# Optimization experiments

Hardware: AMD Instinct MI355X
Metric: run time of the kernel (lower is better)

## Reference

```python
import jax, jax.numpy as jnp
import numpy as np

N = 50000
E = 1600000
D_IN = 64
D_H = 64
D_EMB = 64
D_DEC = 128
B = 4096


def setup_inputs() -> dict:
    key = jax.random.key(0)
    ks = jax.random.split(key, 16)
    def lin(k, fan_in, fan_out):
        return jax.random.normal(k, (fan_in, fan_out), jnp.float32) / np.sqrt(fan_in)
    inp = {
        "x": jax.random.normal(ks[0], (N, D_IN), jnp.float32),
        "edge_index": jax.random.randint(ks[1], (2, E), 0, N),
        "drug_index": jax.random.randint(ks[2], (B, 2), 1, N),
        "bn_gamma": jnp.ones((D_IN,), jnp.float32),
        "bn_beta": jnp.zeros((D_IN,), jnp.float32),
        "Wu1": lin(ks[3], D_IN, D_H), "Wd1": lin(ks[4], D_IN, D_H), "Wb1": lin(ks[5], D_IN, D_H),
        "Wu2": lin(ks[6], 3 * D_H, D_H), "Wd2": lin(ks[7], 3 * D_H, D_H), "Wb2": lin(ks[8], 3 * D_H, D_H),
        "Wu3": lin(ks[9], 3 * D_H, D_EMB), "Wd3": lin(ks[10], 3 * D_H, D_EMB), "Wb3": lin(ks[11], 3 * D_H, D_EMB),
        "P1": jax.random.normal(ks[12], (3 * D_EMB, D_DEC), jnp.float32),
        "P2": jax.random.normal(ks[13], (D_DEC, D_DEC), jnp.float32),
    }
    return inp


def _batchnorm(x, gamma, beta, eps=1e-5):
    mu = jnp.mean(x, axis=0)
    var = jnp.var(x, axis=0)  # biased, matches torch BN training normalization
    return gamma * (x - mu) / jnp.sqrt(var + eps) + beta


def _bgnn_conv(x, row, col, Wu, Wd, Wb, n_nodes):
    # up direction: messages flow row -> col (source_to_target)
    up = x @ Wu
    dn = x @ Wd
    bi = x @ Wb
    ones = jnp.ones(row.shape[0], x.dtype)
    deg_up = jax.ops.segment_sum(ones, col, num_segments=n_nodes)  # in-degree at col
    x_up = jax.ops.segment_sum(up[row] / deg_up[col][:, None], col, num_segments=n_nodes)
    # down direction: flipped edge_index -> messages flow col -> row
    deg_dn = jax.ops.segment_sum(ones, row, num_segments=n_nodes)
    x_dn = jax.ops.segment_sum(dn[col] / deg_dn[row][:, None], row, num_segments=n_nodes)
    c = jnp.concatenate([x_up, x_dn, bi], axis=-1)
    nrm = jnp.linalg.norm(c, axis=-1, keepdims=True)
    return c / jnp.maximum(nrm, 1e-12)


def _leaky(t):
    return jnp.where(t >= 0, t, 0.1 * t)


def reference(x, edge_index, drug_index, bn_gamma, bn_beta,
              Wu1, Wd1, Wb1, Wu2, Wd2, Wb2, Wu3, Wd3, Wb3, P1, P2):
    row, col = edge_index[0], edge_index[1]
    h = _batchnorm(x, bn_gamma, bn_beta)
    h = _leaky(_bgnn_conv(h, row, col, Wu1, Wd1, Wb1, N))
    h = _leaky(_bgnn_conv(h, row, col, Wu2, Wd2, Wb2, N))
    h = _leaky(_bgnn_conv(h, row, col, Wu3, Wd3, Wb3, N))
    di = jnp.reshape(drug_index, (-1, 2))
    a = h[di[:, 0] - 1]  # [B, 3*D_EMB]
    b = h[di[:, 1] - 1]
    M = P1 @ P2 @ P1.T  # [3*D_EMB, 3*D_EMB]
    ypred = jnp.einsum('bd,de,be->b', a, M, b)[:, None]
    return ypred
```

## Files before the change

kernel.cpp:

```cpp
#include <hip/hip_runtime.h>

#define PN 50000
#define PE 1600000
#define PB 4096
#define NP 8
#define PSZ 6250
#define NSW 4
#define SWSZ 12500
#define SCAP 210000
#define CCAP 60000
#define NSL2 4
#define GBLK 2048
#define NPER 7

typedef __attribute__((ext_vector_type(8))) short bf16x8;
typedef __attribute__((ext_vector_type(4))) float f32x4;

__device__ inline float b2f(ushort u) {
    union { unsigned int i; float f; } x; x.i = ((unsigned int)u) << 16; return x.f;
}
__device__ inline ushort f2b(float f) {
    union { float f; unsigned int i; } x; x.f = f;
    unsigned int r = (x.i + 0x7FFFu + ((x.i >> 16) & 1u)) >> 16;
    return (ushort)r;
}

static constexpr size_t L4N = 4 * (size_t)PN;
static constexpr size_t IDXCAP3 = PE + 3 * L4N + 1024;
static constexpr size_t OFF_BN     = 0;
static constexpr size_t OFF_GCUR   = 256;
static constexpr size_t OFF_CCUR   = 272;
static constexpr size_t OFF_TMPM   = 336;
static constexpr size_t OFF_M      = OFF_TMPM + 192 * 128;
static constexpr size_t OFF_WOFFU  = OFF_M + 192 * 192;
static constexpr size_t OFF_WOFFD  = OFF_WOFFU + L4N + 4;
static constexpr size_t OFF_WDEGU  = OFF_WOFFD + L4N + 4;
static constexpr size_t OFF_WDEGD  = OFF_WDEGU + L4N;
static constexpr size_t OFF_PHISTU = OFF_WDEGD + L4N;
static constexpr size_t OFF_PHISTD = OFF_PHISTU + NSL2 * L4N;
static constexpr size_t OFF_IDXU   = OFF_PHISTD + NSL2 * L4N;
static constexpr size_t OFF_IDXD   = OFF_IDXU + (IDXCAP3 + 1) / 2;
static constexpr size_t OFF_STGU   = OFF_IDXD + (IDXCAP3 + 1) / 2;
static constexpr size_t OFF_STGD   = OFF_STGU + NP * (size_t)SCAP;
static constexpr size_t OFF_CHK    = OFF_STGD + NP * (size_t)SCAP;
static constexpr size_t OFF_WB16   = OFF_CHK + 64 * (size_t)CCAP;
static constexpr size_t OFF_HB     = OFF_WB16 + 43008;
static constexpr size_t OFF_PROJ   = OFF_HB + (size_t)PN * 96;

__global__ __launch_bounds__(256) void bn_stats_kernel(const float* __restrict__ x,
                                                       float* __restrict__ sums, int N) {
    __shared__ float ls[256], ls2[256];
    int col = threadIdx.x & 63;
    int rstart = blockIdx.x * 4 + (threadIdx.x >> 6);
    float s = 0.f, s2 = 0.f;
    for (int r = rstart; r < N; r += gridDim.x * 4) {
        float v = x[(size_t)r * 64 + col];
        s += v; s2 += v * v;
    }
    ls[threadIdx.x] = s; ls2[threadIdx.x] = s2;
    __syncthreads();
    if (threadIdx.x < 64) {
        s  = ls[threadIdx.x]  + ls[threadIdx.x + 64]  + ls[threadIdx.x + 128]  + ls[threadIdx.x + 192];
        s2 = ls2[threadIdx.x] + ls2[threadIdx.x + 64] + ls2[threadIdx.x + 128] + ls2[threadIdx.x + 192];
        atomicAdd(&sums[col], s);
        atomicAdd(&sums[64 + col], s2);
    }
}

__global__ __launch_bounds__(64) void bn_finalize_kernel(const float* __restrict__ gamma,
                                                         const float* __restrict__ beta,
                                                         float* __restrict__ bn, int N) {
    int c = threadIdx.x;
    float mean = bn[c] / (float)N;
    float var = bn[64 + c] / (float)N - mean * mean;
    float sc = gamma[c] * rsqrtf(var + 1e-5f);
    bn[128 + c] = sc;
    bn[192 + c] = beta[c] - mean * sc;
}

__global__ __launch_bounds__(256) void bin_kernel(const int* __restrict__ ei,
                                                  int* __restrict__ gcur,
                                                  uint* __restrict__ stgu,
                                                  uint* __restrict__ stgd, int E) {
    __shared__ uint sbuf[16][1024];
    __shared__ int scnt[16], sbase[16];
    const int tid = threadIdx.x;
    for (int base = blockIdx.x * 1024; base < E; base += gridDim.x * 1024) {
        if (tid < 16) scnt[tid] = 0;
        __syncthreads();
#pragma unroll
        for (int j = 0; j < 4; ++j) {
            int e = base + j * 256 + tid;
            if (e < E) {
                int r = __builtin_nontemporal_load(&ei[e]);
                int c = __builtin_nontemporal_load(&ei[E + e]);
                int pu = c / PSZ;
                int slot = atomicAdd(&scnt[pu], 1);
                sbuf[pu][slot] = ((uint)c << 16) | (uint)r;
                int pd = r / PSZ;
                int slot2 = atomicAdd(&scnt[8 + pd], 1);
                sbuf[8 + pd][slot2] = ((uint)r << 16) | (uint)c;
            }
        }
        __syncthreads();
        if (tid < 16) sbase[tid] = atomicAdd(&gcur[tid], scnt[tid]);
        __syncthreads();
#pragma unroll 1
        for (int k = 0; k < 16; ++k) {
            int cnt = scnt[k];
            int gb = sbase[k];
            uint* dst = (k < 8) ? (stgu + (size_t)k * SCAP) : (stgd + (size_t)(k - 8) * SCAP);
            for (int i = tid; i < cnt; i += 256) {
                int gi = gb + i;
                if (gi < SCAP) dst[gi] = sbuf[k][i];
            }
        }
        __syncthreads();
    }
}

__global__ __launch_bounds__(256) void rebin_kernel(const uint* __restrict__ stgu,
                                                    const uint* __restrict__ stgd,
                                                    const int* __restrict__ gcur,
                                                    int* __restrict__ ccur,
                                                    uint* __restrict__ chk) {
    __shared__ uint sb[4][1024];
    __shared__ int sc[4], sbase[4];
    const int p = blockIdx.x & 7;
    const int dir = (blockIdx.x >> 3) & 1;
    const int sl = blockIdx.x >> 4;
    const int tid = threadIdx.x;
    const int cnt = min(gcur[dir * 8 + p], SCAP);
    const uint* stg = (dir ? stgd : stgu) + (size_t)p * SCAP;
    const int cbase = p + dir * 8;
    const int per = (cnt + 7) / 8;
    const int s0 = sl * per, s1 = min(cnt, s0 + per);
    for (int base = s0; base < s1; base += 1024) {
        if (tid < 4) sc[tid] = 0;
        __syncthreads();
#pragma unroll
        for (int j = 0; j < 4; ++j) {
            int i = base + j * 256 + tid;
            if (i < s1) {
                uint u = stg[i];
                int w = (int)(u & 0xFFFFu) / SWSZ;
                int slot = atomicAdd(&sc[w], 1);
                sb[w][slot] = u;
            }
        }
        __syncthreads();
        if (tid < 4) sbase[tid] = atomicAdd(&ccur[cbase + 16 * tid], sc[tid]);
        __syncthreads();
#pragma unroll 1
        for (int k = 0; k < 4; ++k) {
            int ck = sc[k];
            int gb = sbase[k];
            uint* dst = chk + (size_t)(cbase + 16 * k) * CCAP;
            for (int i = tid; i < ck; i += 256) {
                int gi = gb + i;
                if (gi < CCAP) dst[gi] = sb[k][i];
            }
        }
        __syncthreads();
    }
}

__global__ __launch_bounds__(256) void hist_kernel(const uint* __restrict__ chk,
                                                   const int* __restrict__ ccur,
                                                   int* __restrict__ phistu,
                                                   int* __restrict__ phistd) {
    __shared__ int hist[PSZ];
    const int c = blockIdx.x & 63;
    const int s = blockIdx.x >> 6;
    const int p = c & 7;
    const int dir = (c >> 3) & 1;
    const int w = c >> 4;
    const int tid = threadIdx.x;
    const int lo = p * PSZ;
    for (int i = tid; i < PSZ; i += 256) hist[i] = 0;
    __syncthreads();
    const int cnt = min(ccur[c], CCAP);
    const uint* stg = chk + (size_t)c * CCAP;
    const int per = (cnt + NSL2 - 1) / NSL2;
    const int s0 = s * per, s1 = min(cnt, s0 + per);
    for (int i = s0 + tid; i < s1; i += 256)
        atomicAdd(&hist[(int)(stg[i] >> 16) - lo], 1);
    __syncthreads();
    int* ph = (dir ? phistd : phistu) + (size_t)s * L4N;
    for (int i = tid; i < PSZ; i += 256) ph[(size_t)(lo + i) * NSW + w] = hist[i];
}

__global__ __launch_bounds__(1024) void scan_kernel(const int* __restrict__ phA,
                                                    const int* __restrict__ phB,
                                                    int* __restrict__ offA,
                                                    int* __restrict__ offB,
                                                    int* __restrict__ degA,
                                                    int* __restrict__ degB, int len) {
    const int* ph = blockIdx.x ? phB : phA;
    int* off = blockIdx.x ? offB : offA;
    int* dego = blockIdx.x ? degB : degA;
    __shared__ int wsum[17];
    int tid = threadIdx.x, lane = tid & 63, wid = tid >> 6;
    int run = 0;
    for (int base = 0; base < len; base += 4096) {
        int i4 = base + tid * 4;
        int4 v = make_int4(0, 0, 0, 0);
        if (i4 < len) {
#pragma unroll
            for (int sl = 0; sl < NSL2; ++sl) {
                int4 t = *(const int4*)&ph[(size_t)sl * len + i4];
                v.x += t.x; v.y += t.y; v.z += t.z; v.w += t.w;
            }
            *(int4*)&dego[i4] = v;
        }
        v.x = (v.x + 3) & ~3; v.y = (v.y + 3) & ~3;
        v.z = (v.z + 3) & ~3; v.w = (v.w + 3) & ~3;
        int lsum = v.x + v.y + v.z + v.w;
        int inc = lsum;
#pragma unroll
        for (int d = 1; d < 64; d <<= 1) {
            int t = __shfl_up(inc, d);
            if (lane >= d) inc += t;
        }
        if (lane == 63) wsum[wid] = inc;
        __syncthreads();
        if (tid == 0) {
            int r2 = 0;
#pragma unroll
            for (int i = 0; i < 16; ++i) { int t = wsum[i]; wsum[i] = r2; r2 += t; }
            wsum[16] = r2;
        }
        __syncthreads();
        if (i4 < len) {
            int pre = run + wsum[wid] + inc - lsum;
            int4 o;
            o.x = pre; o.y = pre + v.x; o.z = o.y + v.y; o.w = o.z + v.z;
            *(int4*)&off[i4] = o;
        }
        run += wsum[16];
        __syncthreads();
    }
    if (tid == 0) off[len] = run;
}

__global__ __launch_bounds__(256) void scatter_kernel(const uint* __restrict__ chk,
                                                      const int* __restrict__ ccur,
                                                      const int* __restrict__ phistu,
                                                      const int* __restrict__ phistd,
                                                      const int* __restrict__ woffu,
                                                      const int* __restrict__ woffd,
                                                      ushort* __restrict__ idxu,
                                                      ushort* __restrict__ idxd) {
    __shared__ int cur[PSZ];
    const int c = blockIdx.x & 63;
    const int s = blockIdx.x >> 6;
    const int p = c & 7;
    const int dir = (c >> 3) & 1;
    const int w = c >> 4;
    const int tid = threadIdx.x;
    const int lo = p * PSZ;
    const int* woff = (dir ? woffd : woffu);
    const int* phist = (dir ? phistd : phistu);
    for (int i = tid; i < PSZ; i += 256) {
        size_t key = (size_t)(lo + i) * NSW + w;
        int cv = woff[key];
        for (int t = 0; t < s; ++t) cv += phist[(size_t)t * L4N + key];
        cur[i] = cv;
    }
    __syncthreads();
    const int cnt = min(ccur[c], CCAP);
    const uint* stg = chk + (size_t)c * CCAP;
    ushort* idx = (dir ? idxd : idxu);
    const int per = (cnt + NSL2 - 1) / NSL2;
    const int s0 = s * per, s1 = min(cnt, s0 + per);
    for (int i = s0 + tid; i < s1; i += 256) {
        uint u = stg[i];
        int pos = atomicAdd(&cur[(int)(u >> 16) - lo], 1);
        idx[pos] = (ushort)(u & 0xFFFFu);
    }
}

template<int K>
__global__ __launch_bounds__(256) void wconv_kernel(const float* __restrict__ Wu,
                                                    const float* __restrict__ Wd,
                                                    const float* __restrict__ Wb,
                                                    ushort* __restrict__ out) {
    int idx = blockIdx.x * 256 + threadIdx.x;
    if (idx >= 192 * K) return;
    int c = idx / K, k = idx - c * K;
    const float* W = (c < 64) ? Wu : (c < 128 ? Wd : Wb);
    out[idx] = f2b(W[k * 64 + (c & 63)]);
}

template<int K, bool BN>
__global__ __launch_bounds__(256) void gemm_kernel(const ushort* __restrict__ hb,
                                                   const float* __restrict__ x,
                                                   const float* __restrict__ bn,
                                                   const ushort* __restrict__ wb,
                                                   ushort* __restrict__ proj, int nrows) {
    constexpr int KP = K + 8;
    __shared__ ushort wlds[192 * KP];
    const int tid = threadIdx.x;
    constexpr int KB8 = K / 8;
    for (int idx = tid; idx < 192 * KB8; idx += 256) {
        int col = idx / KB8, kb = idx - col * KB8;
        *(bf16x8*)&wlds[col * KP + kb * 8] = *(const bf16x8*)&wb[(size_t)col * K + kb * 8];
    }
    __syncthreads();
    const int lane = tid & 63, wid = tid >> 6;
    const int kgrp = (lane >> 4) * 8;
    const int rbase = blockIdx.x * 128 + wid * 32;
    int ar[2] = { min(rbase + (lane & 15), nrows - 1),
                  min(rbase + 16 + (lane & 15), nrows - 1) };
    f32x4 acc[2][12];
#pragma unroll
    for (int rt = 0; rt < 2; ++rt)
#pragma unroll
        for (int ct = 0; ct < 12; ++ct) acc[rt][ct] = (f32x4)0.0f;

#pragma unroll
    for (int k0 = 0; k0 < K; k0 += 32) {
        bf16x8 af[2];
        if (BN) {
#pragma unroll
            for (int rt = 0; rt < 2; ++rt)
#pragma unroll
                for (int j = 0; j < 8; ++j) {
                    int c = k0 + kgrp + j;
                    float v = x[(size_t)ar[rt] * 64 + c] * bn[128 + c] + bn[192 + c];
                    af[rt][j] = (short)f2b(v);
                }
        } else {
#pragma unroll
            for (int rt = 0; rt < 2; ++rt)
                af[rt] = *(const bf16x8*)&hb[(size_t)ar[rt] * 192 + k0 + kgrp];
        }
#pragma unroll
        for (int ct = 0; ct < 12; ++ct) {
            bf16x8 bfr = *(const bf16x8*)&wlds[(ct * 16 + (lane & 15)) * KP + k0 + kgrp];
            acc[0][ct] = __builtin_amdgcn_mfma_f32_16x16x32_bf16(af[0], bfr, acc[0][ct], 0, 0, 0);
            acc[1][ct] = __builtin_amdgcn_mfma_f32_16x16x32_bf16(af[1], bfr, acc[1][ct], 0, 0, 0);
        }
    }
    const int orow0 = blockIdx.x * 128 + wid * 32 + (lane >> 4) * 4;
#pragma unroll
    for (int rt = 0; rt < 2; ++rt)
#pragma unroll
        for (int ct = 0; ct < 12; ++ct) {
            int ocol = ct * 16 + (lane & 15);
#pragma unroll
            for (int j = 0; j < 4; ++j) {
                int orow = orow0 + rt * 16 + j;
                if (orow < nrows) proj[(size_t)orow * 192 + ocol] = f2b(acc[rt][ct][j]);
            }
        }
}

__global__ __launch_bounds__(256) void gather_kernel(const ushort* __restrict__ proj,
                                                     const int* __restrict__ woffu,
                                                     const int* __restrict__ wdegu,
                                                     const int* __restrict__ woffd,
                                                     const int* __restrict__ wdegd,
                                                     const ushort* __restrict__ idxu,
                                                     const ushort* __restrict__ idxd,
                                                     ushort* __restrict__ hb, int N) {
    const int gw = blockIdx.x * 4 + (threadIdx.x >> 6);
    const int nwaves = gridDim.x * 4;
    const int lane = threadIdx.x & 63;
    const int half = lane >> 5;
    const int sl = lane & 31;
    const int* __restrict__ woff = half ? woffd : woffu;
    const int* __restrict__ wdeg = half ? wdegd : wdegu;
    const ushort* __restrict__ idx = half ? idxd : idxu;
    const uint* __restrict__ rowb = (const uint*)proj + half * 32 + sl;

    float a0[NPER], a1[NPER];
    int dtot[NPER];
#pragma unroll
    for (int j = 0; j < NPER; ++j) { a0[j] = 0.f; a1[j] = 0.f; dtot[j] = 0; }

    for (int w = 0; w < NSW; ++w) {
#pragma unroll
        for (int j = 0; j < NPER; ++j) {
            int n = gw + j * nwaves;
            if (n < N) {
                int key = n * NSW + w;
                int s = woff[key];
                int cnt = wdeg[key];
                dtot[j] += cnt;
                const ushort* p = idx + s;
                for (int i = 0; i < cnt; i += 4) {
                    ushort4 U = *(const ushort4*)(p + i);
                    int v1 = (i + 1 < cnt), v2 = (i + 2 < cnt), v3 = (i + 3 < cnt);
                    int s0 = (int)U.x;
                    int s1 = v1 ? (int)U.y : 0;
                    int s2 = v2 ? (int)U.z : 0;
                    int s3 = v3 ? (int)U.w : 0;
                    uint w0 = rowb[(size_t)s0 * 96];
                    uint w1 = rowb[(size_t)s1 * 96];
                    uint w2 = rowb[(size_t)s2 * 96];
                    uint w3 = rowb[(size_t)s3 * 96];
                    if (!v1) w1 = 0; if (!v2) w2 = 0; if (!v3) w3 = 0;
                    a0[j] += __uint_as_float(w0 << 16) + __uint_as_float(w1 << 16)
                           + __uint_as_float(w2 << 16) + __uint_as_float(w3 << 16);
                    a1[j] += __uint_as_float(w0 & 0xFFFF0000u) + __uint_as_float(w1 & 0xFFFF0000u)
                           + __uint_as_float(w2 & 0xFFFF0000u) + __uint_as_float(w3 & 0xFFFF0000u);
                }
            }
        }
        __syncthreads();
    }

    uint* hb32 = (uint*)hb;
#pragma unroll
    for (int j = 0; j < NPER; ++j) {
        int n = gw + j * nwaves;
        if (n >= N) continue;
        float sc = 1.0f / (float)max(dtot[j], 1);
        float A0 = a0[j] * sc, A1 = a1[j] * sc;
        uint bw = (half == 0) ? ((const uint*)proj)[(size_t)n * 96 + 64 + sl] : 0u;
        float b0 = __uint_as_float(bw << 16);
        float b1 = __uint_as_float(bw & 0xFFFF0000u);
        float ss = A0 * A0 + A1 * A1 + b0 * b0 + b1 * b1;
#pragma unroll
        for (int off = 32; off; off >>= 1) ss += __shfl_xor(ss, off);
        float r = 1.0f / fmaxf(sqrtf(ss), 1e-12f);
        A0 *= r; A1 *= r; b0 *= r; b1 *= r;
        A0 = A0 >= 0.f ? A0 : 0.1f * A0;
        A1 = A1 >= 0.f ? A1 : 0.1f * A1;
        hb32[(size_t)n * 96 + half * 32 + sl] = (uint)f2b(A0) | ((uint)f2b(A1) << 16);
        if (half == 0) {
            b0 = b0 >= 0.f ? b0 : 0.1f * b0;
            b1 = b1 >= 0.f ? b1 : 0.1f * b1;
            hb32[(size_t)n * 96 + 64 + sl] = (uint)f2b(b0) | ((uint)f2b(b1) << 16);
        }
    }
}

__global__ __launch_bounds__(128) void m1_kernel(const float* __restrict__ P1,
                                                 const float* __restrict__ P2,
                                                 float* __restrict__ tmpM) {
    int i = blockIdx.x, c = threadIdx.x;
    float s = 0.f;
    for (int k = 0; k < 128; ++k) s += P1[i * 128 + k] * P2[k * 128 + c];
    tmpM[i * 128 + c] = s;
}

__global__ __launch_bounds__(192) void m2_kernel(const float* __restrict__ tmpM,
                                                 const float* __restrict__ P1,
                                                 float* __restrict__ M) {
    __shared__ float trow[128];
    int i = blockIdx.x, j = threadIdx.x;
    if (j < 128) trow[j] = tmpM[i * 128 + j];
    __syncthreads();
    float s = 0.f;
    for (int k = 0; k < 128; ++k) s += trow[k] * P1[j * 128 + k];
    M[i * 192 + j] = s;
}

__global__ __launch_bounds__(192) void decode_kernel(const ushort* __restrict__ hb,
                                                     const int* __restrict__ di,
                                                     const float* __restrict__ M,
                                                     float* __restrict__ out) {
    __shared__ alignas(16) float bvs[8][192];
    __shared__ float red[3][8];
    int pb = blockIdx.x * 8;
    int i = threadIdx.x;
#pragma unroll
    for (int p = 0; p < 8; ++p) {
        int nb = di[(pb + p) * 2 + 1] - 1;
        bvs[p][i] = b2f(hb[(size_t)nb * 192 + i]);
    }
    __syncthreads();
    float t[8] = {};
    const float4* M4 = (const float4*)(M + (size_t)i * 192);
    for (int j4 = 0; j4 < 48; ++j4) {
        float4 m = M4[j4];
#pragma unroll
        for (int p = 0; p < 8; ++p) {
            float4 b = *(const float4*)&bvs[p][j4 * 4];
            t[p] += m.x * b.x + m.y * b.y + m.z * b.z + m.w * b.w;
        }
    }
    int wid = i >> 6, lane = i & 63;
#pragma unroll
    for (int p = 0; p < 8; ++p) {
        int na = di[(pb + p) * 2] - 1;
        float v = b2f(hb[(size_t)na * 192 + i]) * t[p];
#pragma unroll
        for (int off = 32; off; off >>= 1) v += __shfl_xor(v, off);
        if (lane == 0) red[wid][p] = v;
    }
    __syncthreads();
    if (i < 8) out[pb + i] = red[0][i] + red[1][i] + red[2][i];
}

extern "C" void kernel_launch(void* const* d_in, const int* in_sizes, int n_in,
                              void* d_out, int out_size, void* d_ws, size_t ws_size,
                              hipStream_t stream) {
    const float* x     = (const float*)d_in[0];
    const int*   ei    = (const int*)d_in[1];
    const int*   di    = (const int*)d_in[2];
    const float* gamma = (const float*)d_in[3];
    const float* beta  = (const float*)d_in[4];
    const float* Wu[3] = {(const float*)d_in[5], (const float*)d_in[8],  (const float*)d_in[11]};
    const float* Wd[3] = {(const float*)d_in[6], (const float*)d_in[9],  (const float*)d_in[12]};
    const float* Wb[3] = {(const float*)d_in[7], (const float*)d_in[10], (const float*)d_in[13]};
    const float* P1    = (const float*)d_in[14];
    const float* P2    = (const float*)d_in[15];
    float* out = (float*)d_out;
    float* ws  = (float*)d_ws;

    float* bn    = ws + OFF_BN;
    int* gcur  = (int*)(ws + OFF_GCUR);
    int* ccur  = (int*)(ws + OFF_CCUR);
    float* tmpM  = ws + OFF_TMPM;
    float* M     = ws + OFF_M;
    int* woffu = (int*)(ws + OFF_WOFFU);
    int* woffd = (int*)(ws + OFF_WOFFD);
    int* wdegu = (int*)(ws + OFF_WDEGU);
    int* wdegd = (int*)(ws + OFF_WDEGD);
    int* phistu = (int*)(ws + OFF_PHISTU);
    int* phistd = (int*)(ws + OFF_PHISTD);
    ushort* idxu = (ushort*)(ws + OFF_IDXU);
    ushort* idxd = (ushort*)(ws + OFF_IDXD);
    uint* stgu = (uint*)(ws + OFF_STGU);
    uint* stgd = (uint*)(ws + OFF_STGD);
    uint* chk  = (uint*)(ws + OFF_CHK);
    ushort* wb16 = (ushort*)(ws + OFF_WB16);
    ushort* hb   = (ushort*)(ws + OFF_HB);
    ushort* proj = (ushort*)(ws + OFF_PROJ);
    ushort* wbl[3] = {wb16, wb16 + 12288, wb16 + 49152};

    hipMemsetAsync(ws, 0, 336 * sizeof(float), stream);

    bn_stats_kernel<<<200, 256, 0, stream>>>(x, bn, PN);
    bn_finalize_kernel<<<1, 64, 0, stream>>>(gamma, beta, bn, PN);

    bin_kernel<<<512, 256, 0, stream>>>(ei, gcur, stgu, stgd, PE);
    rebin_kernel<<<128, 256, 0, stream>>>(stgu, stgd, gcur, ccur, chk);
    hist_kernel<<<64 * NSL2, 256, 0, stream>>>(chk, ccur, phistu, phistd);
    scan_kernel<<<2, 1024, 0, stream>>>(phistu, phistd, woffu, woffd, wdegu, wdegd, (int)L4N);
    scatter_kernel<<<64 * NSL2, 256, 0, stream>>>(chk, ccur, phistu, phistd,
                                                  woffu, woffd, idxu, idxd);

    wconv_kernel<64><<<(192 * 64 + 255) / 256, 256, 0, stream>>>(Wu[0], Wd[0], Wb[0], wbl[0]);
    wconv_kernel<192><<<(192 * 192 + 255) / 256, 256, 0, stream>>>(Wu[1], Wd[1], Wb[1], wbl[1]);
    wconv_kernel<192><<<(192 * 192 + 255) / 256, 256, 0, stream>>>(Wu[2], Wd[2], Wb[2], wbl[2]);

    const int ngb = (PN + 127) / 128;
    gemm_kernel<64, true><<<ngb, 256, 0, stream>>>(hb, x, bn, wbl[0], proj, PN);
    gather_kernel<<<GBLK, 256, 0, stream>>>(proj, woffu, wdegu, woffd, wdegd, idxu, idxd, hb, PN);
    gemm_kernel<192, false><<<ngb, 256, 0, stream>>>(hb, x, bn, wbl[1], proj, PN);
    gather_kernel<<<GBLK, 256, 0, stream>>>(proj, woffu, wdegu, woffd, wdegd, idxu, idxd, hb, PN);
    gemm_kernel<192, false><<<ngb, 256, 0, stream>>>(hb, x, bn, wbl[2], proj, PN);
    gather_kernel<<<GBLK, 256, 0, stream>>>(proj, woffu, wdegu, woffd, wdegd, idxu, idxd, hb, PN);

    m1_kernel<<<192, 128, 0, stream>>>(P1, P2, tmpM);
    m2_kernel<<<192, 192, 0, stream>>>(tmpM, P1, M);
    decode_kernel<<<PB / 8, 192, 0, stream>>>(hb, di, M, out);
}
```

Measured before the change: 699.5 us.

## Single-pass edge binning, 8-wide padded gathers, and decode-only final aggregation

Merges the two-pass bin/rebin edge partitioning into one kernel that bins directly into 64 chunk buckets, using a small shared-memory buffer and a direct global atomic fallback on overflow. Pads each per-node index segment to a multiple of 8 with a sentinel node whose projection row is zeroed, so the gather loop reads 8 indices per step without validity masks. The last-layer aggregation now runs only for the nodes referenced by drug_index rather than all N nodes. This removes a staging pass and most of the last gather. In exchange it adds a padfill kernel, more index memory, and contended global atomics when a bucket overflows.

After: 655.2 us. 6.3% less time.

```diff
diff --git a/kernel.cpp b/kernel.cpp
--- a/kernel.cpp
+++ b/kernel.cpp
@@ -7,14 +7,17 @@
 #define PSZ 6250
 #define NSW 4
 #define SWSZ 12500
-#define SCAP 210000
 #define CCAP 60000
+#define BCAP 128
 #define NSL2 4
 #define GBLK 2048
 #define NPER 7
+#define GBLK3 512
+#define NPER3 4
 
 typedef __attribute__((ext_vector_type(8))) short bf16x8;
 typedef __attribute__((ext_vector_type(4))) float f32x4;
+typedef __attribute__((ext_vector_type(8))) unsigned short u16x8;
 
 __device__ inline float b2f(ushort u) {
     union { unsigned int i; float f; } x; x.i = ((unsigned int)u) << 16; return x.f;
@@ -26,10 +29,9 @@
 }
 
 static constexpr size_t L4N = 4 * (size_t)PN;
-static constexpr size_t IDXCAP3 = PE + 3 * L4N + 1024;
+static constexpr size_t IDXCAP = PE + 7 * L4N + 1024;
 static constexpr size_t OFF_BN     = 0;
-static constexpr size_t OFF_GCUR   = 256;
-static constexpr size_t OFF_CCUR   = 272;
+static constexpr size_t OFF_CCUR   = 256;
 static constexpr size_t OFF_TMPM   = 336;
 static constexpr size_t OFF_M      = OFF_TMPM + 192 * 128;
 static constexpr size_t OFF_WOFFU  = OFF_M + 192 * 192;
@@ -39,10 +41,8 @@
 static constexpr size_t OFF_PHISTU = OFF_WDEGD + L4N;
 static constexpr size_t OFF_PHISTD = OFF_PHISTU + NSL2 * L4N;
 static constexpr size_t OFF_IDXU   = OFF_PHISTD + NSL2 * L4N;
-static constexpr size_t OFF_IDXD   = OFF_IDXU + (IDXCAP3 + 1) / 2;
-static constexpr size_t OFF_STGU   = OFF_IDXD + (IDXCAP3 + 1) / 2;
-static constexpr size_t OFF_STGD   = OFF_STGU + NP * (size_t)SCAP;
-static constexpr size_t OFF_CHK    = OFF_STGD + NP * (size_t)SCAP;
+static constexpr size_t OFF_IDXD   = OFF_IDXU + (IDXCAP + 1) / 2;
+static constexpr size_t OFF_CHK    = OFF_IDXD + (IDXCAP + 1) / 2;
 static constexpr size_t OFF_WB16   = OFF_CHK + 64 * (size_t)CCAP;
 static constexpr size_t OFF_HB     = OFF_WB16 + 43008;
 static constexpr size_t OFF_PROJ   = OFF_HB + (size_t)PN * 96;
@@ -79,14 +79,13 @@
 }
 
 __global__ __launch_bounds__(256) void bin_kernel(const int* __restrict__ ei,
-                                                  int* __restrict__ gcur,
-                                                  uint* __restrict__ stgu,
-                                                  uint* __restrict__ stgd, int E) {
-    __shared__ uint sbuf[16][1024];
-    __shared__ int scnt[16], sbase[16];
+                                                  int* __restrict__ ccur,
+                                                  uint* __restrict__ chk, int E) {
+    __shared__ uint sbuf[64][BCAP];
+    __shared__ int scnt[64], sbase[64];
     const int tid = threadIdx.x;
     for (int base = blockIdx.x * 1024; base < E; base += gridDim.x * 1024) {
-        if (tid < 16) scnt[tid] = 0;
+        if (tid < 64) scnt[tid] = 0;
         __syncthreads();
 #pragma unroll
         for (int j = 0; j < 4; ++j) {
@@ -94,71 +93,29 @@
             if (e < E) {
                 int r = __builtin_nontemporal_load(&ei[e]);
                 int c = __builtin_nontemporal_load(&ei[E + e]);
-                int pu = c / PSZ;
-                int slot = atomicAdd(&scnt[pu], 1);
-                sbuf[pu][slot] = ((uint)c << 16) | (uint)r;
-                int pd = r / PSZ;
-                int slot2 = atomicAdd(&scnt[8 + pd], 1);
-                sbuf[8 + pd][slot2] = ((uint)r << 16) | (uint)c;
+                uint uu = ((uint)c << 16) | (uint)r;
+                int cu = c / PSZ + 16 * (r / SWSZ);
+                int slot = atomicAdd(&scnt[cu], 1);
+                if (slot < BCAP) sbuf[cu][slot] = uu;
+                else { int pos = atomicAdd(&ccur[cu], 1); if (pos < CCAP) chk[(size_t)cu * CCAP + pos] = uu; }
+                uint ud = ((uint)r << 16) | (uint)c;
+                int cd = r / PSZ + 8 + 16 * (c / SWSZ);
+                int slot2 = atomicAdd(&scnt[cd], 1);
+                if (slot2 < BCAP) sbuf[cd][slot2] = ud;
+                else { int pos = atomicAdd(&ccur[cd], 1); if (pos < CCAP) chk[(size_t)cd * CCAP + pos] = ud; }
             }
         }
         __syncthreads();
-        if (tid < 16) sbase[tid] = atomicAdd(&gcur[tid], scnt[tid]);
+        if (tid < 64) sbase[tid] = atomicAdd(&ccur[tid], min(scnt[tid], BCAP));
         __syncthreads();
 #pragma unroll 1
-        for (int k = 0; k < 16; ++k) {
-            int cnt = scnt[k];
+        for (int k = 0; k < 64; ++k) {
+            int cnt = min(scnt[k], BCAP);
             int gb = sbase[k];
-            uint* dst = (k < 8) ? (stgu + (size_t)k * SCAP) : (stgd + (size_t)(k - 8) * SCAP);
+            uint* dst = chk + (size_t)k * CCAP;
             for (int i = tid; i < cnt; i += 256) {
                 int gi = gb + i;
-                if (gi < SCAP) dst[gi] = sbuf[k][i];
-            }
-        }
-        __syncthreads();
-    }
-}
-
-__global__ __launch_bounds__(256) void rebin_kernel(const uint* __restrict__ stgu,
-                                                    const uint* __restrict__ stgd,
-                                                    const int* __restrict__ gcur,
-                                                    int* __restrict__ ccur,
-                                                    uint* __restrict__ chk) {
-    __shared__ uint sb[4][1024];
-    __shared__ int sc[4], sbase[4];
-    const int p = blockIdx.x & 7;
-    const int dir = (blockIdx.x >> 3) & 1;
-    const int sl = blockIdx.x >> 4;
-    const int tid = threadIdx.x;
-    const int cnt = min(gcur[dir * 8 + p], SCAP);
-    const uint* stg = (dir ? stgd : stgu) + (size_t)p * SCAP;
-    const int cbase = p + dir * 8;
-    const int per = (cnt + 7) / 8;
-    const int s0 = sl * per, s1 = min(cnt, s0 + per);
-    for (int base = s0; base < s1; base += 1024) {
-        if (tid < 4) sc[tid] = 0;
-        __syncthreads();
-#pragma unroll
-        for (int j = 0; j < 4; ++j) {
-            int i = base + j * 256 + tid;
-            if (i < s1) {
-                uint u = stg[i];
-                int w = (int)(u & 0xFFFFu) / SWSZ;
-                int slot = atomicAdd(&sc[w], 1);
-                sb[w][slot] = u;
-            }
-        }
-        __syncthreads();
-        if (tid < 4) sbase[tid] = atomicAdd(&ccur[cbase + 16 * tid], sc[tid]);
-        __syncthreads();
-#pragma unroll 1
-        for (int k = 0; k < 4; ++k) {
-            int ck = sc[k];
-            int gb = sbase[k];
-            uint* dst = chk + (size_t)(cbase + 16 * k) * CCAP;
-            for (int i = tid; i < ck; i += 256) {
-                int gi = gb + i;
-                if (gi < CCAP) dst[gi] = sb[k][i];
+                if (gi < CCAP) dst[gi] = sbuf[k][i];
             }
         }
         __syncthreads();
@@ -213,8 +170,8 @@
             }
             *(int4*)&dego[i4] = v;
         }
-        v.x = (v.x + 3) & ~3; v.y = (v.y + 3) & ~3;
-        v.z = (v.z + 3) & ~3; v.w = (v.w + 3) & ~3;
+        v.x = (v.x + 7) & ~7; v.y = (v.y + 7) & ~7;
+        v.z = (v.z + 7) & ~7; v.w = (v.w + 7) & ~7;
         int lsum = v.x + v.y + v.z + v.w;
         int inc = lsum;
 #pragma unroll
@@ -280,6 +237,23 @@
     }
 }
 
+__global__ __launch_bounds__(256) void padfill_kernel(const int* __restrict__ woffu,
+                                                      const int* __restrict__ wdegu,
+                                                      const int* __restrict__ woffd,
+                                                      const int* __restrict__ wdegd,
+                                                      ushort* __restrict__ idxu,
+                                                      ushort* __restrict__ idxd) {
+    int k = blockIdx.x * 256 + threadIdx.x;
+    int half = (k >= (int)L4N);
+    if (half) k -= (int)L4N;
+    if (k >= (int)L4N) return;
+    const int* woff = half ? woffd : woffu;
+    const int* wdeg = half ? wdegd : wdegu;
+    ushort* idx = half ? idxd : idxu;
+    int off = woff[k], d = wdeg[k], pe = (d + 7) & ~7;
+    for (int i = d; i < pe; ++i) idx[off + i] = (ushort)PN;
+}
+
 template<int K>
 __global__ __launch_bounds__(256) void wconv_kernel(const float* __restrict__ Wu,
                                                     const float* __restrict__ Wd,
@@ -356,6 +330,7 @@
         }
 }
 
+template<int NPERT, bool DI>
 __global__ __launch_bounds__(256) void gather_kernel(const ushort* __restrict__ proj,
                                                      const int* __restrict__ woffu,
                                                      const int* __restrict__ wdegu,
@@ -363,6 +338,7 @@
                                                      const int* __restrict__ wdegd,
                                                      const ushort* __restrict__ idxu,
                                                      const ushort* __restrict__ idxd,
+                                                     const int* __restrict__ di,
                                                      ushort* __restrict__ hb, int N) {
     const int gw = blockIdx.x * 4 + (threadIdx.x >> 6);
     const int nwaves = gridDim.x * 4;
@@ -374,37 +350,46 @@
     const ushort* __restrict__ idx = half ? idxd : idxu;
     const uint* __restrict__ rowb = (const uint*)proj + half * 32 + sl;
 
-    float a0[NPER], a1[NPER];
-    int dtot[NPER];
-#pragma unroll
-    for (int j = 0; j < NPER; ++j) { a0[j] = 0.f; a1[j] = 0.f; dtot[j] = 0; }
+    int nn[NPERT];
+#pragma unroll
+    for (int j = 0; j < NPERT; ++j) {
+        int k = gw + j * nwaves;
+        nn[j] = DI ? (k < 2 * PB ? di[k] - 1 : -1) : (k < N ? k : -1);
+    }
+    float a0[NPERT], a1[NPERT];
+    int dtot[NPERT];
+#pragma unroll
+    for (int j = 0; j < NPERT; ++j) { a0[j] = 0.f; a1[j] = 0.f; dtot[j] = 0; }
 
     for (int w = 0; w < NSW; ++w) {
 #pragma unroll
-        for (int j = 0; j < NPER; ++j) {
-            int n = gw + j * nwaves;
-            if (n < N) {
+        for (int j = 0; j < NPERT; ++j) {
+            int n = nn[j];
+            if (n >= 0) {
                 int key = n * NSW + w;
                 int s = woff[key];
                 int cnt = wdeg[key];
                 dtot[j] += cnt;
+                int cntp = (cnt + 7) & ~7;
                 const ushort* p = idx + s;
-                for (int i = 0; i < cnt; i += 4) {
-                    ushort4 U = *(const ushort4*)(p + i);
-                    int v1 = (i + 1 < cnt), v2 = (i + 2 < cnt), v3 = (i + 3 < cnt);
-                    int s0 = (int)U.x;
-                    int s1 = v1 ? (int)U.y : 0;
-                    int s2 = v2 ? (int)U.z : 0;
-                    int s3 = v3 ? (int)U.w : 0;
-                    uint w0 = rowb[(size_t)s0 * 96];
-                    uint w1 = rowb[(size_t)s1 * 96];
-                    uint w2 = rowb[(size_t)s2 * 96];
-                    uint w3 = rowb[(size_t)s3 * 96];
-                    if (!v1) w1 = 0; if (!v2) w2 = 0; if (!v3) w3 = 0;
-                    a0[j] += __uint_as_float(w0 << 16) + __uint_as_float(w1 << 16)
-                           + __uint_as_float(w2 << 16) + __uint_as_float(w3 << 16);
-                    a1[j] += __uint_as_float(w0 & 0xFFFF0000u) + __uint_as_float(w1 & 0xFFFF0000u)
-                           + __uint_as_float(w2 & 0xFFFF0000u) + __uint_as_float(w3 & 0xFFFF0000u);
+                for (int i = 0; i < cntp; i += 8) {
+                    u16x8 U = *(const u16x8*)(p + i);
+                    uint w0 = rowb[(size_t)U[0] * 96];
+                    uint w1 = rowb[(size_t)U[1] * 96];
+                    uint w2 = rowb[(size_t)U[2] * 96];
+                    uint w3 = rowb[(size_t)U[3] * 96];
+                    uint w4 = rowb[(size_t)U[4] * 96];
+                    uint w5 = rowb[(size_t)U[5] * 96];
+                    uint w6 = rowb[(size_t)U[6] * 96];
+                    uint w7 = rowb[(size_t)U[7] * 96];
+                    a0[j] += (__uint_as_float(w0 << 16) + __uint_as_float(w1 << 16))
+                           + (__uint_as_float(w2 << 16) + __uint_as_float(w3 << 16))
+                           + (__uint_as_float(w4 << 16) + __uint_as_float(w5 << 16))
+                           + (__uint_as_float(w6 << 16) + __uint_as_float(w7 << 16));
+                    a1[j] += (__uint_as_float(w0 & 0xFFFF0000u) + __uint_as_float(w1 & 0xFFFF0000u))
+                           + (__uint_as_float(w2 & 0xFFFF0000u) + __uint_as_float(w3 & 0xFFFF0000u))
+                           + (__uint_as_float(w4 & 0xFFFF0000u) + __uint_as_float(w5 & 0xFFFF0000u))
+                           + (__uint_as_float(w6 & 0xFFFF0000u) + __uint_as_float(w7 & 0xFFFF0000u));
                 }
             }
         }
@@ -413,9 +398,9 @@
 
     uint* hb32 = (uint*)hb;
 #pragma unroll
-    for (int j = 0; j < NPER; ++j) {
-        int n = gw + j * nwaves;
-        if (n >= N) continue;
+    for (int j = 0; j < NPERT; ++j) {
+        int n = nn[j];
+        if (n < 0) continue;
         float sc = 1.0f / (float)max(dtot[j], 1);
         float A0 = a0[j] * sc, A1 = a1[j] * sc;
         uint bw = (half == 0) ? ((const uint*)proj)[(size_t)n * 96 + 64 + sl] : 0u;
@@ -512,7 +497,6 @@
     float* ws  = (float*)d_ws;
 
     float* bn    = ws + OFF_BN;
-    int* gcur  = (int*)(ws + OFF_GCUR);
     int* ccur  = (int*)(ws + OFF_CCUR);
     float* tmpM  = ws + OFF_TMPM;
     float* M     = ws + OFF_M;
@@ -524,8 +508,6 @@
     int* phistd = (int*)(ws + OFF_PHISTD);
     ushort* idxu = (ushort*)(ws + OFF_IDXU);
     ushort* idxd = (ushort*)(ws + OFF_IDXD);
-    uint* stgu = (uint*)(ws + OFF_STGU);
-    uint* stgd = (uint*)(ws + OFF_STGD);
     uint* chk  = (uint*)(ws + OFF_CHK);
     ushort* wb16 = (ushort*)(ws + OFF_WB16);
     ushort* hb   = (ushort*)(ws + OFF_HB);
@@ -533,16 +515,18 @@
     ushort* wbl[3] = {wb16, wb16 + 12288, wb16 + 49152};
 
     hipMemsetAsync(ws, 0, 336 * sizeof(float), stream);
+    hipMemsetAsync(proj + (size_t)PN * 192, 0, 384, stream);
 
     bn_stats_kernel<<<200, 256, 0, stream>>>(x, bn, PN);
     bn_finalize_kernel<<<1, 64, 0, stream>>>(gamma, beta, bn, PN);
 
-    bin_kernel<<<512, 256, 0, stream>>>(ei, gcur, stgu, stgd, PE);
-    rebin_kernel<<<128, 256, 0, stream>>>(stgu, stgd, gcur, ccur, chk);
+    bin_kernel<<<512, 256, 0, stream>>>(ei, ccur, chk, PE);
     hist_kernel<<<64 * NSL2, 256, 0, stream>>>(chk, ccur, phistu, phistd);
     scan_kernel<<<2, 1024, 0, stream>>>(phistu, phistd, woffu, woffd, wdegu, wdegd, (int)L4N);
     scatter_kernel<<<64 * NSL2, 256, 0, stream>>>(chk, ccur, phistu, phistd,
                                                   woffu, woffd, idxu, idxd);
+    padfill_kernel<<<(2 * (int)L4N + 255) / 256, 256, 0, stream>>>(woffu, wdegu, woffd, wdegd,
+                                                                   idxu, idxd);
 
     wconv_kernel<64><<<(192 * 64 + 255) / 256, 256, 0, stream>>>(Wu[0], Wd[0], Wb[0], wbl[0]);
     wconv_kernel<192><<<(192 * 192 + 255) / 256, 256, 0, stream>>>(Wu[1], Wd[1], Wb[1], wbl[1]);
@@ -550,11 +534,14 @@
 
     const int ngb = (PN + 127) / 128;
     gemm_kernel<64, true><<<ngb, 256, 0, stream>>>(hb, x, bn, wbl[0], proj, PN);
-    gather_kernel<<<GBLK, 256, 0, stream>>>(proj, woffu, wdegu, woffd, wdegd, idxu, idxd, hb, PN);
+    gather_kernel<NPER, false><<<GBLK, 256, 0, stream>>>(proj, woffu, wdegu, woffd, wdegd,
+                                                         idxu, idxd, di, hb, PN);
     gemm_kernel<192, false><<<ngb, 256, 0, stream>>>(hb, x, bn, wbl[1], proj, PN);
-    gather_kernel<<<GBLK, 256, 0, stream>>>(proj, woffu, wdegu, woffd, wdegd, idxu, idxd, hb, PN);
+    gather_kernel<NPER, false><<<GBLK, 256, 0, stream>>>(proj, woffu, wdegu, woffd, wdegd,
+                                                         idxu, idxd, di, hb, PN);
     gemm_kernel<192, false><<<ngb, 256, 0, stream>>>(hb, x, bn, wbl[2], proj, PN);
-    gather_kernel<<<GBLK, 256, 0, stream>>>(proj, woffu, wdegu, woffd, wdegd, idxu, idxd, hb, PN);
+    gather_kernel<NPER3, true><<<GBLK3, 256, 0, stream>>>(proj, woffu, wdegu, woffd, wdegd,
+                                                          idxu, idxd, di, hb, PN);
 
     m1_kernel<<<192, 128, 0, stream>>>(P1, P2, tmpM);
     m2_kernel<<<192, 192, 0, stream>>>(tmpM, P1, M);
```
